# Performance work log

Hardware: AMD Instinct MI355X
Metric: run time of the kernel (lower is better)

Reference implementation:

```python
import jax, jax.numpy as jnp
import numpy as np

N, E = 50000, 800000
IN_DIM, HID, OUT = 512, 128, 64
EPS = 0.3
N_LAYERS = 2


def setup_inputs() -> dict:
    key = jax.random.key(0)
    ks = jax.random.split(key, 10)
    src = jax.random.randint(ks[0], (E,), 0, N, dtype=jnp.int32)
    dst = jax.random.randint(ks[1], (E,), 0, N, dtype=jnp.int32)
    yes_no = jax.random.randint(ks[2], (E,), 0, 2, dtype=jnp.int32)
    # symmetric degree norm d = (deg+1)^-1/2 (self-loop-adjusted, as in DGL FAGCN)
    deg = jax.ops.segment_sum(jnp.ones((E,), jnp.float32), dst, num_segments=N)
    d = jax.lax.rsqrt(deg + 1.0)
    return {
        "h": jax.random.normal(ks[3], (N, IN_DIM), jnp.float32),
        "d": d,
        "t1_w": jax.random.normal(ks[4], (HID, IN_DIM), jnp.float32) * (1.414 / np.sqrt(IN_DIM)),
        "t1_b": jnp.zeros((HID,), jnp.float32),
        "gate_w": jax.random.normal(ks[5], (N_LAYERS, 2 * HID), jnp.float32) * (1.414 / np.sqrt(2 * HID)),
        "gate_b": jnp.zeros((N_LAYERS,), jnp.float32),
        "t2_w": jax.random.normal(ks[6], (OUT, HID), jnp.float32) * (1.414 / np.sqrt(HID)),
        "t2_b": jnp.zeros((OUT,), jnp.float32),
        "yes_weight": jnp.float32(1.5),
        "no_weight": jnp.float32(-0.5),
        "src": src,
        "dst": dst,
        "yes_no": yes_no,
    }


def reference(h, d, t1_w, t1_b, gate_w, gate_b, t2_w, t2_b, yes_weight, no_weight, src, dst, yes_no):
    n = h.shape[0]
    hdim = t1_w.shape[0]
    yn = yes_no.astype(h.dtype)
    # yes/no edge bias is layer-independent
    yn_term = jnp.tanh(yn * yes_weight + (1.0 - yn) * no_weight)  # [E]
    dd = d[dst] * d[src]  # [E]

    x = jax.nn.relu(h @ t1_w.T + t1_b)  # [N, H] (dropout is identity in eval)
    raw = x
    for i in range(gate_w.shape[0]):
        # gate(concat(h_dst, h_src)) == h@w_dst (gathered at dst) + h@w_src (gathered at src)
        gd = x @ gate_w[i, :hdim]   # [N]
        gs = x @ gate_w[i, hdim:]   # [N]
        g = jnp.tanh(gd[dst] + gs[src] + gate_b[i])  # [E]
        e = (g + yn_term) * 0.5 * dd                 # [E]
        msg = x[src] * e[:, None]                    # [E, H]
        z = jax.ops.segment_sum(msg, dst, num_segments=n)  # [N, H]
        x = EPS * raw + z
    logits = x @ t2_w.T + t2_b
    return jax.nn.log_softmax(logits, axis=1)
```

## Files before the change

kernel.cpp:

```cpp
#include <hip/hip_runtime.h>
#include <math.h>

#define N_NODES 50000
#define N_EDGES 800000
#define IN_DIM  512
#define HID     128
#define OUT_DIM 64
#define EPS     0.3f

#define SCAN_BLOCKS 49
#define LDS_ROW 516

typedef __attribute__((ext_vector_type(8))) short bf16x8;
typedef __attribute__((ext_vector_type(8))) __bf16 bf16v8;
typedef __attribute__((ext_vector_type(4))) float f32x4;

__device__ __forceinline__ float fast_tanh(float x) {
    return 1.0f - 2.0f / (__expf(2.0f * x) + 1.0f);
}

__device__ __forceinline__ unsigned short f2bfu(float f) {
    return __builtin_bit_cast(unsigned short, (__bf16)f);
}
__device__ __forceinline__ unsigned pk2(float lo, float hi) {
    return (unsigned)f2bfu(lo) | ((unsigned)f2bfu(hi) << 16);
}
__device__ __forceinline__ float bf_lo(unsigned u) { return __uint_as_float(u << 16); }
__device__ __forceinline__ float bf_hi(unsigned u) { return __uint_as_float(u & 0xffff0000u); }

__device__ __forceinline__ int deg_of(float dv) {
    return (int)(1.0f / (dv * dv) + 0.5f) - 1;
}


__global__ void partial_k(const float* __restrict__ d, int* __restrict__ partials) {
    int base = blockIdx.x * 1024 + threadIdx.x * 4;
    int s = 0;
#pragma unroll
    for (int j = 0; j < 4; j++) if (base + j < N_NODES) s += deg_of(d[base + j]);
#pragma unroll
    for (int off = 32; off; off >>= 1) s += __shfl_down(s, off);
    __shared__ int ws[4];
    int lane = threadIdx.x & 63, wv = threadIdx.x >> 6;
    if (lane == 0) ws[wv] = s;
    __syncthreads();
    if (threadIdx.x == 0) partials[blockIdx.x] = ws[0] + ws[1] + ws[2] + ws[3];
}

__global__ void scanp_k(const int* __restrict__ partials, int* __restrict__ bofs,
                        int* __restrict__ rowptr) {
    if (threadIdx.x == 0) {
        int a = 0;
        for (int i = 0; i < SCAN_BLOCKS; i++) { bofs[i] = a; a += partials[i]; }
        rowptr[N_NODES] = a;
    }
}

__global__ void scanw_k(const float* __restrict__ d, const int* __restrict__ bofs,
                        int* __restrict__ rowptr, int* __restrict__ cursor) {
    int base = blockIdx.x * 1024 + threadIdx.x * 4;
    int v[4]; int s = 0;
#pragma unroll
    for (int j = 0; j < 4; j++) {
        v[j] = (base + j < N_NODES) ? deg_of(d[base + j]) : 0;
        s += v[j];
    }
    int lane = threadIdx.x & 63, wv = threadIdx.x >> 6;
    int sc = s;
#pragma unroll
    for (int off = 1; off < 64; off <<= 1) {
        int t = __shfl_up(sc, off);
        if (lane >= off) sc += t;
    }
    __shared__ int wtot[4];
    if (lane == 63) wtot[wv] = sc;
    __syncthreads();
    int wof = 0;
    for (int w = 0; w < wv; w++) wof += wtot[w];
    int excl = bofs[blockIdx.x] + wof + (sc - s);
#pragma unroll
    for (int j = 0; j < 4; j++) {
        if (base + j < N_NODES) { rowptr[base + j] = excl; cursor[base + j] = excl; }
        excl += v[j];
    }
}

__global__ void fill_k(const int* __restrict__ src, const int* __restrict__ dst,
                       const int* __restrict__ yn, int* __restrict__ cursor,
                       int* __restrict__ csr) {
    int e = blockIdx.x * blockDim.x + threadIdx.x;
    if (e >= N_EDGES) return;
    int pos = atomicAdd(&cursor[dst[e]], 1);
    csr[pos] = src[e] | (yn[e] << 31);
}


__global__ void wb_k(const float* __restrict__ w, unsigned short* __restrict__ wb) {
    int t = blockIdx.x * blockDim.x + threadIdx.x;
    if (t >= 8192) return;
    int lane = t & 63;
    int ct   = (t >> 6) & 7;
    int ks   = t >> 9;
    int row  = ct * 16 + (lane & 15);
    int kb   = ks * 32 + (lane >> 4) * 8;
    const float* p = &w[(size_t)row * IN_DIM + kb];
    float4 v0 = *(const float4*)p, v1 = *(const float4*)(p + 4);
    uint4 pk;
    pk.x = pk2(v0.x, v0.y);
    pk.y = pk2(v0.z, v0.w);
    pk.z = pk2(v1.x, v1.y);
    pk.w = pk2(v1.z, v1.w);
    *(uint4*)&wb[(size_t)t * 8] = pk;
}


__launch_bounds__(256)
__global__ void t1_k(const float* __restrict__ h, const unsigned short* __restrict__ wb,
                     const float* __restrict__ bias, const float* __restrict__ gw0,
                     unsigned short* __restrict__ xb0,
                     float* __restrict__ gd0, float* __restrict__ gs0) {
    __shared__ float At[16 * LDS_ROW];
    __shared__ float red[4][4][4][2];
    int tid  = threadIdx.x;
    int lane = tid & 63;
    int wv   = tid >> 6;
    int l15  = lane & 15;
    int quad = lane >> 4;
    int rowb = blockIdx.x * 16;

#pragma unroll
    for (int i = 0; i < 8; ++i) {
        int c    = wv * 8 + i;
        int row  = c >> 1, half = c & 1;
        const float* gsrc = &h[(size_t)(rowb + row) * IN_DIM + half * 256 + lane * 4];
        float* ldst = &At[row * LDS_ROW + half * 256];
        __builtin_amdgcn_global_load_lds(
            (const __attribute__((address_space(1))) unsigned int*)gsrc,
            (__attribute__((address_space(3))) unsigned int*)ldst, 16, 0, 0);
    }
    __syncthreads();

    int ct0 = wv * 2;
    const unsigned short* bp = &wb[(size_t)lane * 8];
    const float* arp = &At[l15 * LDS_ROW + quad * 8];
    f32x4 acc[2];
    acc[0] = (f32x4){0.f, 0.f, 0.f, 0.f};
    acc[1] = (f32x4){0.f, 0.f, 0.f, 0.f};
#pragma unroll 4
    for (int ks = 0; ks < 16; ++ks) {
        float4 a0 = *(const float4*)(arp + ks * 32);
        float4 a1 = *(const float4*)(arp + ks * 32 + 4);
        bf16v8 av;
        av[0] = (__bf16)a0.x; av[1] = (__bf16)a0.y;
        av[2] = (__bf16)a0.z; av[3] = (__bf16)a0.w;
        av[4] = (__bf16)a1.x; av[5] = (__bf16)a1.y;
        av[6] = (__bf16)a1.z; av[7] = (__bf16)a1.w;
        bf16x8 af = __builtin_bit_cast(bf16x8, av);
        bf16x8 b0 = *(const bf16x8*)(bp + (size_t)(ks * 8 + ct0) * 512);
        bf16x8 b1 = *(const bf16x8*)(bp + (size_t)(ks * 8 + ct0 + 1) * 512);
        acc[0] = __builtin_amdgcn_mfma_f32_16x16x32_bf16(af, b0, acc[0], 0, 0, 0);
        acc[1] = __builtin_amdgcn_mfma_f32_16x16x32_bf16(af, b1, acc[1], 0, 0, 0);
    }

    float pd[4] = {0.f, 0.f, 0.f, 0.f}, ps[4] = {0.f, 0.f, 0.f, 0.f};
#pragma unroll
    for (int ct = 0; ct < 2; ++ct) {
        int o = (ct0 + ct) * 16 + l15;
        float b = bias[o];
        float wd = gw0[o], wsv = gw0[128 + o];
#pragma unroll
        for (int r = 0; r < 4; ++r) {
            float v = acc[ct][r] + b;
            v = v > 0.f ? v : 0.f;
            int node = rowb + quad * 4 + r;
            xb0[(size_t)node * HID + o] = f2bfu(v);
            pd[r] += v * wd; ps[r] += v * wsv;
        }
    }
#pragma unroll
    for (int m = 1; m < 16; m <<= 1) {
#pragma unroll
        for (int r = 0; r < 4; ++r) {
            pd[r] += __shfl_xor(pd[r], m);
            ps[r] += __shfl_xor(ps[r], m);
        }
    }
    if (l15 == 0) {
#pragma unroll
        for (int r = 0; r < 4; ++r) {
            red[wv][quad][r][0] = pd[r];
            red[wv][quad][r][1] = ps[r];
        }
    }
    __syncthreads();
    if (wv == 0 && lane < 16) {
        int q = lane >> 2, r = lane & 3;
        float sd = red[0][q][r][0] + red[1][q][r][0] + red[2][q][r][0] + red[3][q][r][0];
        float ss = red[0][q][r][1] + red[1][q][r][1] + red[2][q][r][1] + red[3][q][r][1];
        gd0[rowb + lane] = sd;
        gs0[rowb + lane] = ss;
    }
}


__global__ void agg_k(const unsigned short* __restrict__ xb,
                      const unsigned short* __restrict__ rb,
                      const int* __restrict__ rowptr, const int* __restrict__ csr,
                      const float* __restrict__ d,
                      const float* __restrict__ gd, const float* __restrict__ gs,
                      const float* __restrict__ gb, int layer,
                      const float* __restrict__ yw, const float* __restrict__ nw,
                      const float* __restrict__ gw_next,
                      float* __restrict__ gd_out, float* __restrict__ gs_out,
                      unsigned short* __restrict__ xb_out) {
    int t = blockIdx.x * blockDim.x + threadIdx.x;
    int nid = t >> 6, lane = t & 63;
    if (nid >= N_NODES) return;
    int l15 = lane & 15, eg = lane >> 4;
    float acc[8];
#pragma unroll
    for (int j = 0; j < 8; j++) acc[j] = 0.f;
    if (lane < 16) {
        uint4 rv = *(const uint4*)&rb[(size_t)nid * HID + l15 * 8];
        acc[0] = EPS * bf_lo(rv.x); acc[1] = EPS * bf_hi(rv.x);
        acc[2] = EPS * bf_lo(rv.y); acc[3] = EPS * bf_hi(rv.y);
        acc[4] = EPS * bf_lo(rv.z); acc[5] = EPS * bf_hi(rv.z);
        acc[6] = EPS * bf_lo(rv.w); acc[7] = EPS * bf_hi(rv.w);
    }
    float gdn = gd[nid] + gb[layer];
    float dn  = d[nid];
    float ty  = fast_tanh(yw[0]);
    float tno = fast_tanh(nw[0]);
    int e0 = rowptr[nid], e1 = rowptr[nid + 1];
    for (int b0 = e0; b0 < e1; b0 += 64) {
        int e = b0 + lane;
        float cf = 0.f; int sidx = 0;
        if (e < e1) {
            int p = csr[e];
            int s = p & 0x7fffffff;
            float ynt = (p < 0) ? ty : tno;
            cf = (fast_tanh(gdn + gs[s]) + ynt) * 0.5f * dn * d[s];
            sidx = s;
        }
        int trips = e1 - b0; if (trips > 64) trips = 64;
        float cfA = __shfl(cf, eg);
        int   sA  = __shfl(sidx, eg);
        uint4 vA  = *(const uint4*)&xb[(size_t)sA * HID + l15 * 8];
        for (int t4 = 0; t4 < trips; t4 += 4) {
            float cfB = 0.f; uint4 vB = make_uint4(0, 0, 0, 0);
            if (t4 + 4 < trips) {
                int nx = t4 + 4 + eg;
                cfB = __shfl(cf, nx);
                int sB = __shfl(sidx, nx);
                vB = *(const uint4*)&xb[(size_t)sB * HID + l15 * 8];
            }
            acc[0] += cfA * bf_lo(vA.x); acc[1] += cfA * bf_hi(vA.x);
            acc[2] += cfA * bf_lo(vA.y); acc[3] += cfA * bf_hi(vA.y);
            acc[4] += cfA * bf_lo(vA.z); acc[5] += cfA * bf_hi(vA.z);
            acc[6] += cfA * bf_lo(vA.w); acc[7] += cfA * bf_hi(vA.w);
            cfA = cfB; vA = vB;
        }
    }
#pragma unroll
    for (int j = 0; j < 8; j++) acc[j] += __shfl_xor(acc[j], 32);
#pragma unroll
    for (int j = 0; j < 8; j++) acc[j] += __shfl_xor(acc[j], 16);
    if (lane < 16) {
        uint4 pk;
        pk.x = pk2(acc[0], acc[1]);
        pk.y = pk2(acc[2], acc[3]);
        pk.z = pk2(acc[4], acc[5]);
        pk.w = pk2(acc[6], acc[7]);
        *(uint4*)&xb_out[(size_t)nid * HID + l15 * 8] = pk;
    }
    if (gw_next) {
        float pd = 0.f, psv = 0.f;
#pragma unroll
        for (int j = 0; j < 8; j++) {
            int o = l15 * 8 + j;
            pd  += acc[j] * gw_next[o];
            psv += acc[j] * gw_next[128 + o];
        }
#pragma unroll
        for (int m = 1; m < 16; m <<= 1) {
            pd  += __shfl_xor(pd, m);
            psv += __shfl_xor(psv, m);
        }
        if (lane == 0) { gd_out[nid] = pd; gs_out[nid] = psv; }
    }
}


__launch_bounds__(256)
__global__ void out_k(const unsigned short* __restrict__ xb, const float* __restrict__ w,
                      const float* __restrict__ bias, float* __restrict__ out) {
    __shared__ float As[64][132];
    __shared__ float Bs[64][132];
    int tid = threadIdx.x;
    int n0  = blockIdx.x * 64;
#pragma unroll
    for (int j = 0; j < 4; j++) {
        int c8 = tid + j * 256;
        int r = c8 >> 4, c = (c8 & 15) * 8;
        int gr = n0 + r;
        uint4 v = make_uint4(0, 0, 0, 0);
        if (gr < N_NODES) v = *(const uint4*)&xb[(size_t)gr * HID + c];
        *(float4*)&As[r][c]     = make_float4(bf_lo(v.x), bf_hi(v.x), bf_lo(v.y), bf_hi(v.y));
        *(float4*)&As[r][c + 4] = make_float4(bf_lo(v.z), bf_hi(v.z), bf_lo(v.w), bf_hi(v.w));
    }
#pragma unroll
    for (int j = 0; j < 8; j++) {
        int f4 = tid + j * 256;
        int r = f4 >> 5, c = (f4 & 31) * 4;
        *(float4*)&Bs[r][c] = *(const float4*)&w[r * HID + c];
    }
    __syncthreads();
    int tn = tid >> 4, to = tid & 15;
    float acc[4][4];
#pragma unroll
    for (int i = 0; i < 4; i++)
#pragma unroll
        for (int j = 0; j < 4; j++) acc[i][j] = 0.0f;
#pragma unroll 2
    for (int k = 0; k < HID; k += 4) {
        float4 av[4], bv[4];
#pragma unroll
        for (int i = 0; i < 4; i++) av[i] = *(const float4*)&As[tn + 16 * i][k];
#pragma unroll
        for (int j = 0; j < 4; j++) bv[j] = *(const float4*)&Bs[to + 16 * j][k];
#pragma unroll
        for (int i = 0; i < 4; i++)
#pragma unroll
            for (int j = 0; j < 4; j++) {
                acc[i][j] += av[i].x * bv[j].x;
                acc[i][j] += av[i].y * bv[j].y;
                acc[i][j] += av[i].z * bv[j].z;
                acc[i][j] += av[i].w * bv[j].w;
            }
    }
    float bj[4];
#pragma unroll
    for (int j = 0; j < 4; j++) bj[j] = bias[to + 16 * j];
#pragma unroll
    for (int i = 0; i < 4; i++) {
        float v[4];
        float m = -1e30f;
#pragma unroll
        for (int j = 0; j < 4; j++) { v[j] = acc[i][j] + bj[j]; m = fmaxf(m, v[j]); }
#pragma unroll
        for (int s = 1; s < 16; s <<= 1) m = fmaxf(m, __shfl_xor(m, s));
        float sum = 0.f;
#pragma unroll
        for (int j = 0; j < 4; j++) sum += __expf(v[j] - m);
#pragma unroll
        for (int s = 1; s < 16; s <<= 1) sum += __shfl_xor(sum, s);
        float lse = m + __logf(sum);
        int r = n0 + tn + 16 * i;
        if (r < N_NODES) {
#pragma unroll
            for (int j = 0; j < 4; j++) out[r * OUT_DIM + to + 16 * j] = v[j] - lse;
        }
    }
}


extern "C" void kernel_launch(void* const* d_in, const int* in_sizes, int n_in,
                              void* d_out, int out_size, void* d_ws, size_t ws_size,
                              hipStream_t stream) {
    const float* h    = (const float*)d_in[0];
    const float* d    = (const float*)d_in[1];
    const float* t1_w = (const float*)d_in[2];
    const float* t1_b = (const float*)d_in[3];
    const float* gw   = (const float*)d_in[4];
    const float* gb   = (const float*)d_in[5];
    const float* t2_w = (const float*)d_in[6];
    const float* t2_b = (const float*)d_in[7];
    const float* yw   = (const float*)d_in[8];
    const float* nw   = (const float*)d_in[9];
    const int* src    = (const int*)d_in[10];
    const int* dst    = (const int*)d_in[11];
    const int* yn     = (const int*)d_in[12];
    float* outp = (float*)d_out;

    char* ws = (char*)d_ws;
    size_t off = 0;
    auto alloc = [&](size_t bytes) {
        void* p = ws + off;
        off = (off + bytes + 255) & ~(size_t)255;
        return p;
    };
    unsigned short* xb0 = (unsigned short*)alloc((size_t)N_NODES * HID * 2);
    unsigned short* xb1 = (unsigned short*)alloc((size_t)N_NODES * HID * 2);
    unsigned short* xb2 = (unsigned short*)alloc((size_t)N_NODES * HID * 2);
    unsigned short* wb  = (unsigned short*)alloc((size_t)8192 * 8 * 2);
    float* gd0    = (float*)alloc((size_t)N_NODES * 4);
    float* gs0    = (float*)alloc((size_t)N_NODES * 4);
    float* gd1    = (float*)alloc((size_t)N_NODES * 4);
    float* gs1    = (float*)alloc((size_t)N_NODES * 4);
    int*   rowptr = (int*)alloc((size_t)(N_NODES + 1) * 4);
    int*   cursor = (int*)alloc((size_t)N_NODES * 4);
    int*   csr    = (int*)alloc((size_t)N_EDGES * 4);
    int*   partials = (int*)alloc(64 * 4);
    int*   bofs     = (int*)alloc(64 * 4);
    (void)ws_size; (void)n_in; (void)in_sizes; (void)out_size;

    partial_k<<<SCAN_BLOCKS, 256, 0, stream>>>(d, partials);
    scanp_k<<<1, 64, 0, stream>>>(partials, bofs, rowptr);
    scanw_k<<<SCAN_BLOCKS, 256, 0, stream>>>(d, bofs, rowptr, cursor);
    fill_k<<<(N_EDGES + 255) / 256, 256, 0, stream>>>(src, dst, yn, cursor, csr);

    wb_k<<<32, 256, 0, stream>>>(t1_w, wb);
    t1_k<<<N_NODES / 16, 256, 0, stream>>>(h, wb, t1_b, gw, xb0, gd0, gs0);

    int wave_blocks = (N_NODES * 64 + 255) / 256;

    agg_k<<<wave_blocks, 256, 0, stream>>>(xb0, xb0, rowptr, csr, d, gd0, gs0, gb, 0,
                                           yw, nw, gw + 256, gd1, gs1, xb1);
    agg_k<<<wave_blocks, 256, 0, stream>>>(xb1, xb0, rowptr, csr, d, gd1, gs1, gb, 1,
                                           yw, nw, (const float*)nullptr,
                                           (float*)nullptr, (float*)nullptr, xb2);

    out_k<<<(N_NODES + 63) / 64, 256, 0, stream>>>(xb2, t2_w, t2_b, outp);
}
```

Measured before the change: 340.5 us.

## Precompute per-edge coefficients in a separate kernel and deepen aggregation prefetch

Moves the per-edge gate coefficient (tanh of gate sums, yes/no term, degree norms) out of the aggregation kernel into a new edge-parallel coef_k kernel, run once per layer. To support that, fill_k now also stores the destination of each CSR slot. The aggregation loop drops the 64-edge coalesced batch and shuffles, and instead runs a three-deep software pipeline that loads csr, coef and the gathered feature row for each group of 4 edges. This removes the coefficient math and its gathers from the latency-bound aggregation loop. In exchange it adds two extra kernel launches, extra writes and reads of per-edge arrays, and narrower uncoalesced index loads on the aggregation critical path.

```diff
diff --git a/kernel.cpp b/kernel.cpp
--- a/kernel.cpp
+++ b/kernel.cpp
@@ -87,11 +87,30 @@
 
 __global__ void fill_k(const int* __restrict__ src, const int* __restrict__ dst,
                        const int* __restrict__ yn, int* __restrict__ cursor,
-                       int* __restrict__ csr) {
+                       int* __restrict__ csr, int* __restrict__ dstp) {
     int e = blockIdx.x * blockDim.x + threadIdx.x;
     if (e >= N_EDGES) return;
-    int pos = atomicAdd(&cursor[dst[e]], 1);
-    csr[pos] = src[e] | (yn[e] << 31);
+    int dv = dst[e];
+    int pos = atomicAdd(&cursor[dv], 1);
+    csr[pos]  = src[e] | (yn[e] << 31);
+    dstp[pos] = dv;
+}
+
+__global__ void coef_k(const int* __restrict__ csr, const int* __restrict__ dstp,
+                       const float* __restrict__ d,
+                       const float* __restrict__ gd, const float* __restrict__ gs,
+                       const float* __restrict__ gb, int layer,
+                       const float* __restrict__ yw, const float* __restrict__ nw,
+                       float* __restrict__ coef) {
+    int e = blockIdx.x * blockDim.x + threadIdx.x;
+    if (e >= N_EDGES) return;
+    int p = csr[e];
+    int s = p & 0xffff;
+    int dn = dstp[e];
+    float ty  = fast_tanh(yw[0]);
+    float tno = fast_tanh(nw[0]);
+    float ynt = (p < 0) ? ty : tno;
+    coef[e] = (fast_tanh(gd[dn] + gs[s] + gb[layer]) + ynt) * 0.5f * d[dn] * d[s];
 }
 
 
@@ -206,10 +225,7 @@
 __global__ void agg_k(const unsigned short* __restrict__ xb,
                       const unsigned short* __restrict__ rb,
                       const int* __restrict__ rowptr, const int* __restrict__ csr,
-                      const float* __restrict__ d,
-                      const float* __restrict__ gd, const float* __restrict__ gs,
-                      const float* __restrict__ gb, int layer,
-                      const float* __restrict__ yw, const float* __restrict__ nw,
+                      const float* __restrict__ coef,
                       const float* __restrict__ gw_next,
                       float* __restrict__ gd_out, float* __restrict__ gs_out,
                       unsigned short* __restrict__ xb_out) {
@@ -227,39 +243,30 @@
         acc[4] = EPS * bf_lo(rv.z); acc[5] = EPS * bf_hi(rv.z);
         acc[6] = EPS * bf_lo(rv.w); acc[7] = EPS * bf_hi(rv.w);
     }
-    float gdn = gd[nid] + gb[layer];
-    float dn  = d[nid];
-    float ty  = fast_tanh(yw[0]);
-    float tno = fast_tanh(nw[0]);
     int e0 = rowptr[nid], e1 = rowptr[nid + 1];
-    for (int b0 = e0; b0 < e1; b0 += 64) {
-        int e = b0 + lane;
-        float cf = 0.f; int sidx = 0;
-        if (e < e1) {
-            int p = csr[e];
-            int s = p & 0x7fffffff;
-            float ynt = (p < 0) ? ty : tno;
-            cf = (fast_tanh(gdn + gs[s]) + ynt) * 0.5f * dn * d[s];
-            sidx = s;
-        }
-        int trips = e1 - b0; if (trips > 64) trips = 64;
-        float cfA = __shfl(cf, eg);
-        int   sA  = __shfl(sidx, eg);
-        uint4 vA  = *(const uint4*)&xb[(size_t)sA * HID + l15 * 8];
-        for (int t4 = 0; t4 < trips; t4 += 4) {
-            float cfB = 0.f; uint4 vB = make_uint4(0, 0, 0, 0);
-            if (t4 + 4 < trips) {
-                int nx = t4 + 4 + eg;
-                cfB = __shfl(cf, nx);
-                int sB = __shfl(sidx, nx);
-                vB = *(const uint4*)&xb[(size_t)sB * HID + l15 * 8];
-            }
-            acc[0] += cfA * bf_lo(vA.x); acc[1] += cfA * bf_hi(vA.x);
-            acc[2] += cfA * bf_lo(vA.y); acc[3] += cfA * bf_hi(vA.y);
-            acc[4] += cfA * bf_lo(vA.z); acc[5] += cfA * bf_hi(vA.z);
-            acc[6] += cfA * bf_lo(vA.w); acc[7] += cfA * bf_hi(vA.w);
-            cfA = cfB; vA = vB;
-        }
+    int nt = (e1 - e0 + 3) >> 2;
+
+    auto fetch = [&](int tt, float& cf, int& s) {
+        int e = e0 + tt * 4 + eg;
+        cf = 0.f; s = 0;
+        if (e < e1) { int p = csr[e]; cf = coef[e]; s = p & 0xffff; }
+    };
+    auto ldx = [&](int s) {
+        return *(const uint4*)&xb[(size_t)s * HID + l15 * 8];
+    };
+
+    float cf0, cf1, cf2; int s0, s1, s2;
+    fetch(0, cf0, s0); fetch(1, cf1, s1); fetch(2, cf2, s2);
+    uint4 v0 = ldx(s0), v1 = ldx(s1), v2 = ldx(s2);
+    for (int tt = 0; tt < nt; tt++) {
+        acc[0] += cf0 * bf_lo(v0.x); acc[1] += cf0 * bf_hi(v0.x);
+        acc[2] += cf0 * bf_lo(v0.y); acc[3] += cf0 * bf_hi(v0.y);
+        acc[4] += cf0 * bf_lo(v0.z); acc[5] += cf0 * bf_hi(v0.z);
+        acc[6] += cf0 * bf_lo(v0.w); acc[7] += cf0 * bf_hi(v0.w);
+        cf0 = cf1; v0 = v1; s0 = s1;
+        cf1 = cf2; v1 = v2; s1 = s2;
+        fetch(tt + 3, cf2, s2);
+        v2 = ldx(s2);
     }
 #pragma unroll
     for (int j = 0; j < 8; j++) acc[j] += __shfl_xor(acc[j], 32);
@@ -400,6 +407,8 @@
     int*   rowptr = (int*)alloc((size_t)(N_NODES + 1) * 4);
     int*   cursor = (int*)alloc((size_t)N_NODES * 4);
     int*   csr    = (int*)alloc((size_t)N_EDGES * 4);
+    int*   dstp   = (int*)alloc((size_t)N_EDGES * 4);
+    float* coef   = (float*)alloc((size_t)N_EDGES * 4);
     int*   partials = (int*)alloc(64 * 4);
     int*   bofs     = (int*)alloc(64 * 4);
     (void)ws_size; (void)n_in; (void)in_sizes; (void)out_size;
@@ -407,17 +416,20 @@
     partial_k<<<SCAN_BLOCKS, 256, 0, stream>>>(d, partials);
     scanp_k<<<1, 64, 0, stream>>>(partials, bofs, rowptr);
     scanw_k<<<SCAN_BLOCKS, 256, 0, stream>>>(d, bofs, rowptr, cursor);
-    fill_k<<<(N_EDGES + 255) / 256, 256, 0, stream>>>(src, dst, yn, cursor, csr);
+    fill_k<<<(N_EDGES + 255) / 256, 256, 0, stream>>>(src, dst, yn, cursor, csr, dstp);
 
     wb_k<<<32, 256, 0, stream>>>(t1_w, wb);
     t1_k<<<N_NODES / 16, 256, 0, stream>>>(h, wb, t1_b, gw, xb0, gd0, gs0);
 
     int wave_blocks = (N_NODES * 64 + 255) / 256;
-
-    agg_k<<<wave_blocks, 256, 0, stream>>>(xb0, xb0, rowptr, csr, d, gd0, gs0, gb, 0,
-                                           yw, nw, gw + 256, gd1, gs1, xb1);
-    agg_k<<<wave_blocks, 256, 0, stream>>>(xb1, xb0, rowptr, csr, d, gd1, gs1, gb, 1,
-                                           yw, nw, (const float*)nullptr,
+    int edge_blocks = (N_EDGES + 255) / 256;
+
+    coef_k<<<edge_blocks, 256, 0, stream>>>(csr, dstp, d, gd0, gs0, gb, 0, yw, nw, coef);
+    agg_k<<<wave_blocks, 256, 0, stream>>>(xb0, xb0, rowptr, csr, coef,
+                                           gw + 256, gd1, gs1, xb1);
+    coef_k<<<edge_blocks, 256, 0, stream>>>(csr, dstp, d, gd1, gs1, gb, 1, yw, nw, coef);
+    agg_k<<<wave_blocks, 256, 0, stream>>>(xb1, xb0, rowptr, csr, coef,
+                                           (const float*)nullptr,
                                            (float*)nullptr, (float*)nullptr, xb2);
 
     out_k<<<(N_NODES + 63) / 64, 256, 0, stream>>>(xb2, t2_w, t2_b, outp);
```

Measured after the change: 373.9 us. +9.8%, slower.
